# Optimization experiments

Hardware: AMD Instinct MI355X
Metric: run time of the kernel (lower is better)

Reference implementation:

```python
import jax, jax.numpy as jnp
import numpy as np

N = 50000      # nodes per graph batch (per side)
E = 600000     # edges per side
B = 4096       # number of graphs (drug pairs)
D = 128        # node_dim == hidden_dim
K = 128        # kge_dim
R = 86         # rel_total
L = 3          # n_iter
EPS = 1e-5


def setup_inputs() -> dict:
    key = jax.random.key(0)
    ks = jax.random.split(key, 16)
    inp = {}
    inp["x1"] = jax.random.normal(ks[0], (N, D), jnp.float32)
    inp["x2"] = jax.random.normal(ks[1], (N, D), jnp.float32)
    inp["edge_index1"] = jax.random.randint(ks[2], (2, E), 0, N)
    inp["edge_index2"] = jax.random.randint(ks[3], (2, E), 0, N)
    inp["batch1"] = jnp.sort(jax.random.randint(ks[4], (N,), 0, B))
    inp["batch2"] = jnp.sort(jax.random.randint(ks[5], (N,), 0, B))
    inp["rel"] = jax.random.randint(ks[6], (B,), 0, R)
    # SAGEConv params, stacked over L layers (all [D,D] since node_dim==hidden_dim)
    sc = 0.05
    inp["Wl"] = jax.random.normal(ks[7], (L, D, D), jnp.float32) * sc   # lin on aggregated neighbors (has bias)
    inp["bl"] = jnp.zeros((L, D), jnp.float32)
    inp["Wr"] = jax.random.normal(ks[8], (L, D, D), jnp.float32) * sc   # root (self) lin, no bias
    # BatchNorm (eval mode: running stats)
    inp["bn_gamma"] = jnp.ones((L, D), jnp.float32)
    inp["bn_beta"] = jnp.zeros((L, D), jnp.float32)
    inp["bn_mean"] = jnp.zeros((L, D), jnp.float32)
    inp["bn_var"] = jnp.ones((L, D), jnp.float32)
    # relation embedding + final MLP
    inp["kge"] = jax.random.normal(ks[9], (R, K), jnp.float32)
    inp["W1"] = jax.random.normal(ks[10], (2 * D + K, D), jnp.float32) * sc
    inp["b1"] = jnp.zeros((D,), jnp.float32)
    inp["W2"] = jax.random.normal(ks[11], (D, 1), jnp.float32) * sc
    inp["b2"] = jnp.zeros((1,), jnp.float32)
    return inp


def _gnn(x, edge_index, Wl, bl, Wr, g, b, m, v):
    src, dst = edge_index[0], edge_index[1]
    deg = jax.ops.segment_sum(jnp.ones((E,), x.dtype), dst, num_segments=N)
    deg = jnp.maximum(deg, 1.0)[:, None]
    for i in range(L):
        agg = jax.ops.segment_sum(x[src], dst, num_segments=N) / deg  # mean aggregation
        h = agg @ Wl[i] + bl[i] + x @ Wr[i]                           # SAGEConv
        h = (h - m[i]) * (g[i] / jnp.sqrt(v[i] + EPS)) + b[i]         # BN (eval)
        x = jax.nn.relu(h)                                            # dropout = identity (eval)
    return x


def reference(x1, edge_index1, batch1, x2, edge_index2, batch2, rel,
              Wl, bl, Wr, bn_gamma, bn_beta, bn_mean, bn_var,
              kge, W1, b1, W2, b2):
    h1 = _gnn(x1, edge_index1, Wl, bl, Wr, bn_gamma, bn_beta, bn_mean, bn_var)
    h2 = _gnn(x2, edge_index2, Wl, bl, Wr, bn_gamma, bn_beta, bn_mean, bn_var)
    p1 = jax.ops.segment_sum(h1, batch1, num_segments=B)  # global_add_pool
    p2 = jax.ops.segment_sum(h2, batch2, num_segments=B)
    r = kge[rel]                                          # [B, K]
    z = jnp.concatenate([p1, p2, r], axis=-1)             # [B, 2D+K]
    h = jax.nn.relu(z @ W1 + b1)
    out = h @ W2 + b2
    return out.reshape(-1)
```

## Files before the change

### kernel.cpp

```cpp
#include <hip/hip_runtime.h>

#define NN 50000
#define NE 600000
#define NB 4096
#define DD 128
#define EPSV 1e-5f
#define NBKT 196
#define NCHUNK 256
#define CHSZ ((NE + NCHUNK - 1) / NCHUNK)

typedef __bf16 bf16x8 __attribute__((ext_vector_type(8)));
typedef float f32x4 __attribute__((ext_vector_type(4)));
typedef float f32x2 __attribute__((ext_vector_type(2)));

__device__ inline unsigned short f2bf(float f) {
    unsigned u = __float_as_uint(f);
    u = (u + 0x7FFFu + ((u >> 16) & 1u)) >> 16;
    return (unsigned short)u;
}
__device__ inline float bf2f(unsigned short h) {
    return __uint_as_float(((unsigned)h) << 16);
}

__global__ void k_prep(const float* __restrict__ x1, const float* __restrict__ x2,
                       unsigned short* __restrict__ xh, unsigned short* __restrict__ xl,
                       const float* __restrict__ Wl, const float* __restrict__ Wr,
                       const float* __restrict__ W1,
                       unsigned short* __restrict__ wf, unsigned* __restrict__ w1p,
                       const int* __restrict__ d0, const int* __restrict__ d1,
                       int* __restrict__ bcnt) {
    __shared__ int h[NBKT];
    int b = blockIdx.x;
    int tid = threadIdx.x;
    if (b < 12500) {
        int i = b * 256 + tid;
        const float* x = (i < NN * 32) ? x1 : x2;
        int j = (i < NN * 32) ? i : i - NN * 32;
        float4 v = ((const float4*)x)[j];
        ushort4 hh, ll;
        hh.x = f2bf(v.x); ll.x = f2bf(v.x - bf2f(hh.x));
        hh.y = f2bf(v.y); ll.y = f2bf(v.y - bf2f(hh.y));
        hh.z = f2bf(v.z); ll.z = f2bf(v.z - bf2f(hh.z));
        hh.w = f2bf(v.w); ll.w = f2bf(v.w - bf2f(hh.w));
        ((ushort4*)xh)[i] = hh;
        ((ushort4*)xl)[i] = ll;
    } else if (b < 12500 + 576) {
        int t = (b - 12500) * 256 + tid;
        if (t < 3 * 128 * 256) {
            int k = t & 255;
            int n = (t >> 8) & 127;
            int l = t >> 15;
            float w = (k < 128) ? Wl[l * 16384 + k * 128 + n] : Wr[l * 16384 + (k - 128) * 128 + n];
            unsigned short hh = f2bf(w);
            unsigned short lo = f2bf(w - bf2f(hh));
            int ntile = n >> 4, fm = n & 15, kc = k >> 5, kq = (k & 31) >> 3, j = k & 7;
            size_t pos = (size_t)l * 65536 + (size_t)(ntile * 8 + kc) * 1024 +
                         (size_t)(kq * 16 + fm) * 8 + j;
            wf[pos] = hh;
            wf[pos + 512] = lo;
        } else if (t < 3 * 128 * 256 + 128 * 384) {
            int u = t - 3 * 128 * 256;
            int n = u / 384;
            int k = u - n * 384;
            float w = W1[k * 128 + n];
            unsigned short hh = f2bf(w);
            unsigned short ll = f2bf(w - bf2f(hh));
            w1p[u] = ((unsigned)hh << 16) | (unsigned)ll;
        }
    } else {
        int hb = b - 13076;
        int side = (hb >= NCHUNK) ? 1 : 0;
        int c = hb - side * NCHUNK;
        const int* dst = side ? d1 : d0;
        for (int i = tid; i < NBKT; i += 256) h[i] = 0;
        __syncthreads();
        int e0 = c * CHSZ, e1 = min(e0 + CHSZ, NE);
        for (int e = e0 + tid; e < e1; e += 256) atomicAdd(&h[dst[e] >> 8], 1);
        __syncthreads();
        int* bc = bcnt + ((size_t)side * NCHUNK + c) * NBKT;
        for (int i = tid; i < NBKT; i += 256) bc[i] = h[i];
    }
}

__global__ void k_s1(int* __restrict__ bcnt, int* __restrict__ btot) {
    int side = (blockIdx.x >= NBKT) ? 1 : 0;
    int b = blockIdx.x - side * NBKT;
    int tid = threadIdx.x;
    int idx = ((size_t)side * NCHUNK + tid) * NBKT + b;
    int v = bcnt[idx];
    int lane = tid & 63, wv = tid >> 6;
    int x = v;
#pragma unroll
    for (int off = 1; off < 64; off <<= 1) {
        int y = __shfl_up(x, off, 64);
        if (lane >= off) x += y;
    }
    __shared__ int ws4[4];
    if (lane == 63) ws4[wv] = x;
    __syncthreads();
    int add = 0;
#pragma unroll
    for (int w = 0; w < 4; w++)
        if (w < wv) add += ws4[w];
    int incl = x + add;
    bcnt[idx] = incl - v;
    if (tid == 255) btot[side * NBKT + b] = incl;
}

__global__ void k_s2(const int* __restrict__ btot, int* __restrict__ bbase,
                     int* __restrict__ ptrC) {
    int side = blockIdx.x;
    int tid = threadIdx.x;
    int v = (tid < NBKT) ? btot[side * NBKT + tid] : 0;
    int lane = tid & 63, wv = tid >> 6;
    int x = v;
#pragma unroll
    for (int off = 1; off < 64; off <<= 1) {
        int y = __shfl_up(x, off, 64);
        if (lane >= off) x += y;
    }
    __shared__ int ws4[4];
    if (lane == 63) ws4[wv] = x;
    __syncthreads();
    int add = 0;
#pragma unroll
    for (int w = 0; w < 4; w++)
        if (w < wv) add += ws4[w];
    int incl = x + add;
    if (tid < NBKT) bbase[side * NBKT + tid] = incl - v;
    if (tid == 0 && side == 1) ptrC[2 * NN] = 2 * NE;
}

__global__ void k_part(const int* __restrict__ s0, const int* __restrict__ d0,
                       const int* __restrict__ s1, const int* __restrict__ d1,
                       const int* __restrict__ bcnt, const int* __restrict__ bbase,
                       int* __restrict__ part) {
    int side = (blockIdx.x >= NCHUNK) ? 1 : 0;
    int c = blockIdx.x - side * NCHUNK;
    const int* src = side ? s1 : s0;
    const int* dst = side ? d1 : d0;
    int tid = threadIdx.x;
    __shared__ int off[NBKT];
    const int* bc = bcnt + ((size_t)side * NCHUNK + c) * NBKT;
    for (int i = tid; i < NBKT; i += 256) off[i] = bbase[side * NBKT + i] + bc[i];
    __syncthreads();
    int e0 = c * CHSZ, e1 = min(e0 + CHSZ, NE);
    int* P = part + (size_t)side * NE;
    int soff = side * NN;
    for (int e = e0 + tid; e < e1; e += 256) {
        int d = dst[e];
        int pos = atomicAdd(&off[d >> 8], 1);
        P[pos] = ((src[e] + soff) << 8) | (d & 255);
    }
}

__global__ void k_csr(const int* __restrict__ part, const int* __restrict__ bbase,
                      int* __restrict__ ptrC, float* __restrict__ invdC,
                      int* __restrict__ csrC) {
    int side = (blockIdx.x >= NBKT) ? 1 : 0;
    int b = blockIdx.x - side * NBKT;
    int tid = threadIdx.x;
    const int* P = part + (size_t)side * NE;
    int base = bbase[side * NBKT + b];
    int endp = (b == NBKT - 1) ? NE : bbase[side * NBKT + b + 1];
    __shared__ int cnt[256];
    cnt[tid] = 0;
    __syncthreads();
    for (int e = base + tid; e < endp; e += 256) atomicAdd(&cnt[P[e] & 255], 1);
    __syncthreads();
    int v = cnt[tid];
    int lane = tid & 63, wv = tid >> 6;
    int x = v;
#pragma unroll
    for (int off = 1; off < 64; off <<= 1) {
        int y = __shfl_up(x, off, 64);
        if (lane >= off) x += y;
    }
    __shared__ int ws4[4];
    if (lane == 63) ws4[wv] = x;
    __syncthreads();
    int add = 0;
#pragma unroll
    for (int w = 0; w < 4; w++)
        if (w < wv) add += ws4[w];
    int excl = x + add - v;
    int node = (b << 8) + tid;
    if (node < NN) {
        ptrC[side * NN + node] = side * NE + base + excl;
        invdC[side * NN + node] = 1.0f / (float)(v > 1 ? v : 1);
    }
    __syncthreads();
    cnt[tid] = excl;
    __syncthreads();
    for (int e = base + tid; e < endp; e += 256) {
        int p = P[e];
        int pos = atomicAdd(&cnt[p & 255], 1);
        csrC[(size_t)side * NE + base + pos] = p >> 8;
    }
}

__global__ void k_gather(const unsigned short* __restrict__ xh, const int* __restrict__ ptr,
                         const int* __restrict__ csr, const float* __restrict__ invd,
                         unsigned short* __restrict__ aggH) {
    int wid = threadIdx.x >> 6;
    int lane = threadIdx.x & 63;
    int q = lane >> 4;
    int c = lane & 15;
    int n = blockIdx.x * 4 + wid;
    if (n >= 2 * NN) return;
    int beg = ptr[n], end = ptr[n + 1];
    float id = invd[n];
    f32x2 a2[4];
#pragma unroll
    for (int k = 0; k < 4; k++) a2[k] = (f32x2){0.f, 0.f};

    for (int base = beg; base < end; base += 64) {
        int cnt = min(end - base, 64);
        int idxv = csr[base + min(lane, cnt - 1)];
        for (int e0 = 0; e0 < cnt; e0 += 16) {
            int eA = e0 + q, eB = e0 + 4 + q, eC = e0 + 8 + q, eD = e0 + 12 + q;
            int iA = __shfl(idxv, eA, 64);
            int iB = __shfl(idxv, eB, 64);
            int iC = __shfl(idxv, eC, 64);
            int iD = __shfl(idxv, eD, 64);
            f32x2 wA2 = (eA < cnt) ? (f32x2){1.f, 1.f} : (f32x2){0.f, 0.f};
            f32x2 wB2 = (eB < cnt) ? (f32x2){1.f, 1.f} : (f32x2){0.f, 0.f};
            f32x2 wC2 = (eC < cnt) ? (f32x2){1.f, 1.f} : (f32x2){0.f, 0.f};
            f32x2 wD2 = (eD < cnt) ? (f32x2){1.f, 1.f} : (f32x2){0.f, 0.f};
            uint4 vA = *(const uint4*)(xh + (((unsigned)iA << 7) + (c << 3)));
            uint4 vB = *(const uint4*)(xh + (((unsigned)iB << 7) + (c << 3)));
            uint4 vC = *(const uint4*)(xh + (((unsigned)iC << 7) + (c << 3)));
            uint4 vD = *(const uint4*)(xh + (((unsigned)iD << 7) + (c << 3)));
            a2[0] += wA2 * (f32x2){__uint_as_float(vA.x << 16), __uint_as_float(vA.x & 0xffff0000u)};
            a2[1] += wA2 * (f32x2){__uint_as_float(vA.y << 16), __uint_as_float(vA.y & 0xffff0000u)};
            a2[2] += wA2 * (f32x2){__uint_as_float(vA.z << 16), __uint_as_float(vA.z & 0xffff0000u)};
            a2[3] += wA2 * (f32x2){__uint_as_float(vA.w << 16), __uint_as_float(vA.w & 0xffff0000u)};
            a2[0] += wB2 * (f32x2){__uint_as_float(vB.x << 16), __uint_as_float(vB.x & 0xffff0000u)};
            a2[1] += wB2 * (f32x2){__uint_as_float(vB.y << 16), __uint_as_float(vB.y & 0xffff0000u)};
            a2[2] += wB2 * (f32x2){__uint_as_float(vB.z << 16), __uint_as_float(vB.z & 0xffff0000u)};
            a2[3] += wB2 * (f32x2){__uint_as_float(vB.w << 16), __uint_as_float(vB.w & 0xffff0000u)};
            a2[0] += wC2 * (f32x2){__uint_as_float(vC.x << 16), __uint_as_float(vC.x & 0xffff0000u)};
            a2[1] += wC2 * (f32x2){__uint_as_float(vC.y << 16), __uint_as_float(vC.y & 0xffff0000u)};
            a2[2] += wC2 * (f32x2){__uint_as_float(vC.z << 16), __uint_as_float(vC.z & 0xffff0000u)};
            a2[3] += wC2 * (f32x2){__uint_as_float(vC.w << 16), __uint_as_float(vC.w & 0xffff0000u)};
            a2[0] += wD2 * (f32x2){__uint_as_float(vD.x << 16), __uint_as_float(vD.x & 0xffff0000u)};
            a2[1] += wD2 * (f32x2){__uint_as_float(vD.y << 16), __uint_as_float(vD.y & 0xffff0000u)};
            a2[2] += wD2 * (f32x2){__uint_as_float(vD.z << 16), __uint_as_float(vD.z & 0xffff0000u)};
            a2[3] += wD2 * (f32x2){__uint_as_float(vD.w << 16), __uint_as_float(vD.w & 0xffff0000u)};
        }
    }
    float a[8];
    a[0] = a2[0][0]; a[1] = a2[0][1];
    a[2] = a2[1][0]; a[3] = a2[1][1];
    a[4] = a2[2][0]; a[5] = a2[2][1];
    a[6] = a2[3][0]; a[7] = a2[3][1];
#pragma unroll
    for (int k = 0; k < 8; k++) {
        a[k] += __shfl_xor(a[k], 16, 64);
        a[k] += __shfl_xor(a[k], 32, 64);
    }
    if (q == 0) {
        unsigned short h0 = f2bf(a[0] * id), h1 = f2bf(a[1] * id);
        unsigned short h2 = f2bf(a[2] * id), h3 = f2bf(a[3] * id);
        unsigned short h4 = f2bf(a[4] * id), h5 = f2bf(a[5] * id);
        unsigned short h6 = f2bf(a[6] * id), h7 = f2bf(a[7] * id);
        uint4 o;
        o.x = (unsigned)h0 | ((unsigned)h1 << 16);
        o.y = (unsigned)h2 | ((unsigned)h3 << 16);
        o.z = (unsigned)h4 | ((unsigned)h5 << 16);
        o.w = (unsigned)h6 | ((unsigned)h7 << 16);
        *(uint4*)(aggH + (size_t)n * DD + c * 8) = o;
    }
}

__launch_bounds__(256)
__global__ void k_gemmW(const unsigned short* __restrict__ AH,
                        const unsigned short* __restrict__ XH, const unsigned short* __restrict__ XL,
                        const unsigned short* __restrict__ wf,
                        const float* __restrict__ bl, const float* __restrict__ g,
                        const float* __restrict__ be, const float* __restrict__ mn,
                        const float* __restrict__ vr,
                        unsigned short* __restrict__ OH, unsigned short* __restrict__ OL,
                        float* __restrict__ Of, int f32out) {
    __shared__ __align__(16) unsigned short sBuf[8192];
    int tid = threadIdx.x;
    int lane = tid & 63, w = tid >> 6;
    int fm = lane & 15, kq = lane >> 4;
    int m0 = blockIdx.x * 64;
    int wr = (w & 1) * 32;
    int wn = (w >> 1) * 64;
    int ksw = kq ^ ((fm >> 1) & 3);

    int srow = tid >> 2, sseg = tid & 3;
    int ldsoff = srow * 32 + ((sseg ^ ((srow >> 1) & 3)) << 3);
    bool sok = (m0 + srow) < 2 * NN;
    size_t gbase = (size_t)(m0 + srow) * DD + sseg * 8;

    float scv[4], shv[4];
#pragma unroll
    for (int nt = 0; nt < 4; nt++) {
        int jj = wn + nt * 16 + fm;
        float s = g[jj] * rsqrtf(vr[jj] + EPSV);
        scv[nt] = s;
        shv[nt] = (bl[jj] - mn[jj]) * s + be[jj];
    }

    f32x4 acc[2][4];
#pragma unroll
    for (int i = 0; i < 2; i++)
#pragma unroll
        for (int j = 0; j < 4; j++) acc[i][j] = (f32x4){0.f, 0.f, 0.f, 0.f};

    const unsigned short* wfb = wf + (size_t)((w >> 1) * 4) * 8192 + lane * 8;

#pragma unroll
    for (int c = 0; c < 8; c++) {
        int isA = (c < 4);
        if (c > 0) __syncthreads();
        {
            uint4 av = make_uint4(0, 0, 0, 0), lv = make_uint4(0, 0, 0, 0);
            size_t gofs = gbase + (size_t)(c & 3) * 32;
            if (sok) {
                av = *(const uint4*)((isA ? AH : XH) + gofs);
                if (!isA) lv = *(const uint4*)(XL + gofs);
            }
            *(uint4*)&sBuf[ldsoff] = av;
            if (!isA) *(uint4*)&sBuf[2048 + ldsoff] = lv;
        }
        bf16x8 wh[4], wl[4];
#pragma unroll
        for (int nt = 0; nt < 4; nt++) {
            const unsigned short* p = wfb + (size_t)(nt * 8 + c) * 1024;
            wh[nt] = *(const bf16x8*)p;
            wl[nt] = *(const bf16x8*)(p + 512);
        }
        __syncthreads();

        bf16x8 ah[2], al[2];
#pragma unroll
        for (int mt = 0; mt < 2; mt++) {
            int r = wr + mt * 16 + fm;
            ah[mt] = *(const bf16x8*)&sBuf[r * 32 + ksw * 8];
            if (!isA) al[mt] = *(const bf16x8*)&sBuf[2048 + r * 32 + ksw * 8];
        }
#pragma unroll
        for (int nt = 0; nt < 4; nt++) {
#pragma unroll
            for (int mt = 0; mt < 2; mt++) {
                acc[mt][nt] = __builtin_amdgcn_mfma_f32_16x16x32_bf16(ah[mt], wh[nt], acc[mt][nt], 0, 0, 0);
                acc[mt][nt] = __builtin_amdgcn_mfma_f32_16x16x32_bf16(ah[mt], wl[nt], acc[mt][nt], 0, 0, 0);
                if (!isA)
                    acc[mt][nt] = __builtin_amdgcn_mfma_f32_16x16x32_bf16(al[mt], wh[nt], acc[mt][nt], 0, 0, 0);
            }
        }
    }

    unsigned* cb = (unsigned*)sBuf;
    int c8 = tid & 15;
    for (int h = 0; h < 2; h++) {
        __syncthreads();
        if ((w & 1) == h) {
#pragma unroll
            for (int mt = 0; mt < 2; mt++) {
#pragma unroll
                for (int r = 0; r < 4; r++) {
                    int rh = mt * 16 + kq * 4 + r;
#pragma unroll
                    for (int nt = 0; nt < 4; nt++) {
                        int col = wn + nt * 16 + fm;
                        float o = fmaxf(acc[mt][nt][r] * scv[nt] + shv[nt], 0.f);
                        unsigned pv;
                        if (f32out) {
                            pv = __float_as_uint(o);
                        } else {
                            unsigned short hi_ = f2bf(o);
                            pv = ((unsigned)hi_ << 16) | (unsigned)f2bf(o - bf2f(hi_));
                        }
                        cb[rh * 128 + col] = pv;
                    }
                }
            }
        }
        __syncthreads();
        if (f32out) {
#pragma unroll
            for (int j = 0; j < 4; j++) {
                int row = (tid >> 5) + j * 8;
                int grow = m0 + h * 32 + row;
                if (grow < 2 * NN)
                    *(uint4*)&Of[(size_t)grow * DD + (tid & 31) * 4] =
                        *(const uint4*)&cb[row * 128 + (tid & 31) * 4];
            }
        } else {
#pragma unroll
            for (int j = 0; j < 2; j++) {
                int row = (tid >> 4) + j * 16;
                int grow = m0 + h * 32 + row;
                if (grow < 2 * NN) {
                    const unsigned* u = &cb[row * 128 + c8 * 8];
                    uint4 hv, lv2;
                    hv.x = (u[0] >> 16) | (u[1] & 0xFFFF0000u);
                    hv.y = (u[2] >> 16) | (u[3] & 0xFFFF0000u);
                    hv.z = (u[4] >> 16) | (u[5] & 0xFFFF0000u);
                    hv.w = (u[6] >> 16) | (u[7] & 0xFFFF0000u);
                    lv2.x = (u[0] & 0xFFFFu) | (u[1] << 16);
                    lv2.y = (u[2] & 0xFFFFu) | (u[3] << 16);
                    lv2.z = (u[4] & 0xFFFFu) | (u[5] << 16);
                    lv2.w = (u[6] & 0xFFFFu) | (u[7] << 16);
                    *(uint4*)&OH[(size_t)grow * DD + c8 * 8] = hv;
                    *(uint4*)&OL[(size_t)grow * DD + c8 * 8] = lv2;
                }
            }
        }
    }
}

__launch_bounds__(128)
__global__ void k_pool2z(const float* __restrict__ cf, const int* __restrict__ bt1,
                         const int* __restrict__ bt2, const int* __restrict__ rel,
                         const float* __restrict__ kge,
                         unsigned short* __restrict__ zh, unsigned short* __restrict__ zl) {
    int side = (blockIdx.x >= NB) ? 1 : 0;
    int b = blockIdx.x - side * NB;
    const int* batch = side ? bt2 : bt1;
    const float* h = cf + (size_t)side * NN * DD;
    __shared__ int sr[2];
    if (threadIdx.x < 2) {
        int target = b + (int)threadIdx.x;
        int lo = 0, hi = NN;
        while (lo < hi) {
            int mid = (lo + hi) >> 1;
            if (batch[mid] < target) lo = mid + 1; else hi = mid;
        }
        sr[threadIdx.x] = lo;
    }
    __syncthreads();
    int beg = sr[0], end = sr[1];
    int t = threadIdx.x;
    float acc = 0.f;
    for (int r = beg; r < end; r++) acc += h[(size_t)r * DD + t];
    size_t zo = (size_t)b * 384 + side * 128 + t;
    unsigned short hh = f2bf(acc);
    zh[zo] = hh;
    zl[zo] = f2bf(acc - bf2f(hh));
    if (side == 0) {
        float kv = kge[(size_t)rel[b] * 128 + t];
        size_t zk = (size_t)b * 384 + 256 + t;
        unsigned short kh = f2bf(kv);
        zh[zk] = kh;
        zl[zk] = f2bf(kv - bf2f(kh));
    }
}

__launch_bounds__(256)
__global__ void k_mlp2(const unsigned short* __restrict__ zh, const unsigned short* __restrict__ zl,
                       const unsigned* __restrict__ w1p,
                       const float* __restrict__ b1, const float* __restrict__ W2,
                       const float* __restrict__ b2, float* __restrict__ out) {
    __shared__ __align__(16) unsigned short sZ[2][32 * 40];
    __shared__ __align__(16) unsigned short sW[2][128 * 40];
    __shared__ float hpart[32][4];
    int tid = threadIdx.x;
    int m0 = blockIdx.x * 32;
    int lane = tid & 63, w = tid >> 6;
    int fm = lane & 15, q = lane >> 4;
    int wn = w * 32;

    f32x4 acc[2][2];
#pragma unroll
    for (int i = 0; i < 2; i++)
#pragma unroll
        for (int j = 0; j < 2; j++) acc[i][j] = (f32x4){0.f, 0.f, 0.f, 0.f};

    for (int c = 0; c < 12; c++) {
        int k0 = c * 32;
        __syncthreads();
        {
            int row = tid >> 3, seg = tid & 7;
            size_t off = (size_t)(m0 + row) * 384 + k0 + seg * 4;
            *(ushort4*)&sZ[0][row * 40 + seg * 4] = *(const ushort4*)(zh + off);
            *(ushort4*)&sZ[1][row * 40 + seg * 4] = *(const ushort4*)(zl + off);
        }
#pragma unroll
        for (int i = 0; i < 4; i++) {
            int u = tid + 256 * i;
            int row = u >> 3, seg = u & 7;
            uint4 val = *(const uint4*)(w1p + (size_t)row * 384 + k0 + seg * 4);
            ushort4 hi, lo;
            hi.x = val.x >> 16; hi.y = val.y >> 16; hi.z = val.z >> 16; hi.w = val.w >> 16;
            lo.x = val.x & 0xFFFF; lo.y = val.y & 0xFFFF; lo.z = val.z & 0xFFFF; lo.w = val.w & 0xFFFF;
            *(ushort4*)&sW[0][row * 40 + seg * 4] = hi;
            *(ushort4*)&sW[1][row * 40 + seg * 4] = lo;
        }
        __syncthreads();
        bf16x8 zfh[2], zfl[2];
#pragma unroll
        for (int mt = 0; mt < 2; mt++) {
            int r = mt * 16 + fm;
            zfh[mt] = *(const bf16x8*)&sZ[0][r * 40 + q * 8];
            zfl[mt] = *(const bf16x8*)&sZ[1][r * 40 + q * 8];
        }
#pragma unroll
        for (int nt = 0; nt < 2; nt++) {
            int nr = wn + nt * 16 + fm;
            bf16x8 wh = *(const bf16x8*)&sW[0][nr * 40 + q * 8];
            bf16x8 wl = *(const bf16x8*)&sW[1][nr * 40 + q * 8];
#pragma unroll
            for (int mt = 0; mt < 2; mt++) {
                acc[mt][nt] = __builtin_amdgcn_mfma_f32_16x16x32_bf16(zfh[mt], wh, acc[mt][nt], 0, 0, 0);
                acc[mt][nt] = __builtin_amdgcn_mfma_f32_16x16x32_bf16(zfh[mt], wl, acc[mt][nt], 0, 0, 0);
                acc[mt][nt] = __builtin_amdgcn_mfma_f32_16x16x32_bf16(zfl[mt], wh, acc[mt][nt], 0, 0, 0);
            }
        }
    }

    float b1v[2], w2v[2];
#pragma unroll
    for (int nt = 0; nt < 2; nt++) {
        int col = wn + nt * 16 + fm;
        b1v[nt] = b1[col];
        w2v[nt] = W2[col];
    }
#pragma unroll
    for (int mt = 0; mt < 2; mt++) {
#pragma unroll
        for (int r = 0; r < 4; r++) {
            float val = 0.f;
#pragma unroll
            for (int nt = 0; nt < 2; nt++)
                val += fmaxf(acc[mt][nt][r] + b1v[nt], 0.f) * w2v[nt];
#pragma unroll
            for (int m = 1; m < 16; m <<= 1) val += __shfl_xor(val, m, 64);
            if (fm == 0) hpart[mt * 16 + q * 4 + r][w] = val;
        }
    }
    __syncthreads();
    if (tid < 32)
        out[m0 + tid] = hpart[tid][0] + hpart[tid][1] + hpart[tid][2] + hpart[tid][3] + b2[0];
}

extern "C" void kernel_launch(void* const* d_in, const int* in_sizes, int n_in,
                              void* d_out, int out_size, void* d_ws, size_t ws_size,
                              hipStream_t stream) {
    const float* x1  = (const float*)d_in[0];
    const float* x2  = (const float*)d_in[1];
    const int*   ei1 = (const int*)d_in[2];
    const int*   ei2 = (const int*)d_in[3];
    const int*   bt1 = (const int*)d_in[4];
    const int*   bt2 = (const int*)d_in[5];
    const int*   rel = (const int*)d_in[6];
    const float* Wl  = (const float*)d_in[7];
    const float* bl  = (const float*)d_in[8];
    const float* Wr  = (const float*)d_in[9];
    const float* g   = (const float*)d_in[10];
    const float* be  = (const float*)d_in[11];
    const float* mn  = (const float*)d_in[12];
    const float* vr  = (const float*)d_in[13];
    const float* kge = (const float*)d_in[14];
    const float* W1  = (const float*)d_in[15];
    const float* b1v = (const float*)d_in[16];
    const float* W2  = (const float*)d_in[17];
    const float* b2v = (const float*)d_in[18];

    char* ws = (char*)d_ws;
    size_t off = 0;
    auto alloc = [&](size_t bytes) {
        void* p = ws + off;
        off += (bytes + 255) & ~(size_t)255;
        return p;
    };
    const size_t PL = (size_t)2 * NN * DD;
    unsigned short* xbufH = (unsigned short*)alloc(PL * 2);
    unsigned short* xbufL = (unsigned short*)alloc(PL * 2);
    unsigned short* obufH = (unsigned short*)alloc(PL * 2);
    unsigned short* obufL = (unsigned short*)alloc(PL * 2);
    unsigned short* aggH  = (unsigned short*)alloc(PL * 2);
    unsigned short* wf    = (unsigned short*)alloc((size_t)3 * 65536 * 2);
    unsigned* w1p  = (unsigned*)alloc((size_t)128 * 384 * 4);
    unsigned short* zh = (unsigned short*)alloc((size_t)NB * 384 * 2);
    unsigned short* zl = (unsigned short*)alloc((size_t)NB * 384 * 2);
    int*   bcnt    = (int*)alloc((size_t)2 * NCHUNK * NBKT * 4);
    int*   btot    = (int*)alloc((size_t)2 * NBKT * 4);
    int*   bbase   = (int*)alloc((size_t)2 * NBKT * 4);
    int*   part    = (int*)alloc((size_t)2 * NE * 4);
    int*   ptrC    = (int*)alloc((size_t)(2 * NN + 1) * 4);
    float* invdC   = (float*)alloc((size_t)2 * NN * 4);
    int*   csrC    = (int*)alloc((size_t)2 * NE * 4);
    if (off > ws_size) return;

    float* cf = (float*)obufH;

    const int nbPrep  = 12500 + 576 + 512;
    const int nbNode4 = (2 * NN + 3) / 4;
    const int nbGemmW = (2 * NN + 63) / 64;

    k_prep<<<nbPrep, 256, 0, stream>>>(x1, x2, xbufH, xbufL, Wl, Wr, W1, wf, w1p,
                                       ei1 + NE, ei2 + NE, bcnt);

    k_s1<<<2 * NBKT, 256, 0, stream>>>(bcnt, btot);
    k_s2<<<2, 256, 0, stream>>>(btot, bbase, ptrC);
    k_part<<<2 * NCHUNK, 256, 0, stream>>>(ei1, ei1 + NE, ei2, ei2 + NE, bcnt, bbase, part);
    k_csr<<<2 * NBKT, 256, 0, stream>>>(part, bbase, ptrC, invdC, csrC);

    k_gather<<<nbNode4, 256, 0, stream>>>(xbufH, ptrC, csrC, invdC, aggH);
    k_gemmW<<<nbGemmW, 256, 0, stream>>>(aggH, xbufH, xbufL, wf, bl, g, be, mn, vr,
                                         obufH, obufL, (float*)nullptr, 0);
    k_gather<<<nbNode4, 256, 0, stream>>>(obufH, ptrC, csrC, invdC, aggH);
    k_gemmW<<<nbGemmW, 256, 0, stream>>>(aggH, obufH, obufL, wf + 65536, bl + 128, g + 128,
                                         be + 128, mn + 128, vr + 128,
                                         xbufH, xbufL, (float*)nullptr, 0);
    k_gather<<<nbNode4, 256, 0, stream>>>(xbufH, ptrC, csrC, invdC, aggH);
    k_gemmW<<<nbGemmW, 256, 0, stream>>>(aggH, xbufH, xbufL, wf + 131072, bl + 256, g + 256,
                                         be + 256, mn + 256, vr + 256,
                                         (unsigned short*)nullptr, (unsigned short*)nullptr, cf, 1);

    k_pool2z<<<2 * NB, 128, 0, stream>>>(cf, bt1, bt2, rel, kge, zh, zl);
    k_mlp2<<<NB / 32, 256, 0, stream>>>(zh, zl, w1p, b1v, W2, b2v, (float*)d_out);
}
```

Measured before the change: 420.3 us.

## Software-pipeline gather loads and widen GEMM LDS staging to 64-wide K chunks

The neighbor gather loop now prefetches the next group of four bf16 rows while it accumulates the current group, so global-load latency overlaps with the unpack-and-add work. The SAGE GEMM kernel stages 64 K-columns per LDS pass instead of 32, using a new 8-way XOR swizzle. This halves the number of barrier-separated stages from 8 to 4. The cost is more live registers in the gather kernel and double the LDS footprint per stage, which could lower occupancy.

```diff
diff --git a/kernel.cpp b/kernel.cpp
--- a/kernel.cpp
+++ b/kernel.cpp
@@ -199,6 +199,32 @@
     }
 }
 
+#define ONE2 ((f32x2){1.f, 1.f})
+#define ZERO2 ((f32x2){0.f, 0.f})
+#define UNP2H(u) __uint_as_float((u) << 16)
+#define UNP2L(u) __uint_as_float((u) & 0xffff0000u)
+#define LOADG(E0, VA, VB, VC, VD, WA, WB, WC, WD)                                  \
+    {                                                                              \
+        int eA_ = (E0) + q, eB_ = (E0) + 4 + q, eC_ = (E0) + 8 + q, eD_ = (E0) + 12 + q; \
+        int iA_ = __shfl(idxv, eA_, 64);                                           \
+        int iB_ = __shfl(idxv, eB_, 64);                                           \
+        int iC_ = __shfl(idxv, eC_, 64);                                           \
+        int iD_ = __shfl(idxv, eD_, 64);                                           \
+        WA = (eA_ < cnt) ? ONE2 : ZERO2;                                           \
+        WB = (eB_ < cnt) ? ONE2 : ZERO2;                                           \
+        WC = (eC_ < cnt) ? ONE2 : ZERO2;                                           \
+        WD = (eD_ < cnt) ? ONE2 : ZERO2;                                           \
+        VA = *(const uint4*)(xh + (((unsigned)iA_ << 7) + (c << 3)));              \
+        VB = *(const uint4*)(xh + (((unsigned)iB_ << 7) + (c << 3)));              \
+        VC = *(const uint4*)(xh + (((unsigned)iC_ << 7) + (c << 3)));              \
+        VD = *(const uint4*)(xh + (((unsigned)iD_ << 7) + (c << 3)));              \
+    }
+#define PROC1(V, W)                                                                \
+    a2[0] += W * (f32x2){UNP2H(V.x), UNP2L(V.x)};                                  \
+    a2[1] += W * (f32x2){UNP2H(V.y), UNP2L(V.y)};                                  \
+    a2[2] += W * (f32x2){UNP2H(V.z), UNP2L(V.z)};                                  \
+    a2[3] += W * (f32x2){UNP2H(V.w), UNP2L(V.w)};
+
 __global__ void k_gather(const unsigned short* __restrict__ xh, const int* __restrict__ ptr,
                          const int* __restrict__ csr, const float* __restrict__ invd,
                          unsigned short* __restrict__ aggH) {
@@ -212,41 +238,25 @@
     float id = invd[n];
     f32x2 a2[4];
 #pragma unroll
-    for (int k = 0; k < 4; k++) a2[k] = (f32x2){0.f, 0.f};
+    for (int k = 0; k < 4; k++) a2[k] = ZERO2;
 
     for (int base = beg; base < end; base += 64) {
         int cnt = min(end - base, 64);
         int idxv = csr[base + min(lane, cnt - 1)];
+        uint4 cA, cB, cC, cD, nA, nB, nC, nD;
+        f32x2 xA, xB, xC, xD, yA, yB, yC, yD;
+        LOADG(0, cA, cB, cC, cD, xA, xB, xC, xD);
         for (int e0 = 0; e0 < cnt; e0 += 16) {
-            int eA = e0 + q, eB = e0 + 4 + q, eC = e0 + 8 + q, eD = e0 + 12 + q;
-            int iA = __shfl(idxv, eA, 64);
-            int iB = __shfl(idxv, eB, 64);
-            int iC = __shfl(idxv, eC, 64);
-            int iD = __shfl(idxv, eD, 64);
-            f32x2 wA2 = (eA < cnt) ? (f32x2){1.f, 1.f} : (f32x2){0.f, 0.f};
-            f32x2 wB2 = (eB < cnt) ? (f32x2){1.f, 1.f} : (f32x2){0.f, 0.f};
-            f32x2 wC2 = (eC < cnt) ? (f32x2){1.f, 1.f} : (f32x2){0.f, 0.f};
-            f32x2 wD2 = (eD < cnt) ? (f32x2){1.f, 1.f} : (f32x2){0.f, 0.f};
-            uint4 vA = *(const uint4*)(xh + (((unsigned)iA << 7) + (c << 3)));
-            uint4 vB = *(const uint4*)(xh + (((unsigned)iB << 7) + (c << 3)));
-            uint4 vC = *(const uint4*)(xh + (((unsigned)iC << 7) + (c << 3)));
-            uint4 vD = *(const uint4*)(xh + (((unsigned)iD << 7) + (c << 3)));
-            a2[0] += wA2 * (f32x2){__uint_as_float(vA.x << 16), __uint_as_float(vA.x & 0xffff0000u)};
-            a2[1] += wA2 * (f32x2){__uint_as_float(vA.y << 16), __uint_as_float(vA.y & 0xffff0000u)};
-            a2[2] += wA2 * (f32x2){__uint_as_float(vA.z << 16), __uint_as_float(vA.z & 0xffff0000u)};
-            a2[3] += wA2 * (f32x2){__uint_as_float(vA.w << 16), __uint_as_float(vA.w & 0xffff0000u)};
-            a2[0] += wB2 * (f32x2){__uint_as_float(vB.x << 16), __uint_as_float(vB.x & 0xffff0000u)};
-            a2[1] += wB2 * (f32x2){__uint_as_float(vB.y << 16), __uint_as_float(vB.y & 0xffff0000u)};
-            a2[2] += wB2 * (f32x2){__uint_as_float(vB.z << 16), __uint_as_float(vB.z & 0xffff0000u)};
-            a2[3] += wB2 * (f32x2){__uint_as_float(vB.w << 16), __uint_as_float(vB.w & 0xffff0000u)};
-            a2[0] += wC2 * (f32x2){__uint_as_float(vC.x << 16), __uint_as_float(vC.x & 0xffff0000u)};
-            a2[1] += wC2 * (f32x2){__uint_as_float(vC.y << 16), __uint_as_float(vC.y & 0xffff0000u)};
-            a2[2] += wC2 * (f32x2){__uint_as_float(vC.z << 16), __uint_as_float(vC.z & 0xffff0000u)};
-            a2[3] += wC2 * (f32x2){__uint_as_float(vC.w << 16), __uint_as_float(vC.w & 0xffff0000u)};
-            a2[0] += wD2 * (f32x2){__uint_as_float(vD.x << 16), __uint_as_float(vD.x & 0xffff0000u)};
-            a2[1] += wD2 * (f32x2){__uint_as_float(vD.y << 16), __uint_as_float(vD.y & 0xffff0000u)};
-            a2[2] += wD2 * (f32x2){__uint_as_float(vD.z << 16), __uint_as_float(vD.z & 0xffff0000u)};
-            a2[3] += wD2 * (f32x2){__uint_as_float(vD.w << 16), __uint_as_float(vD.w & 0xffff0000u)};
+            bool more = (e0 + 16) < cnt;
+            if (more) LOADG(e0 + 16, nA, nB, nC, nD, yA, yB, yC, yD);
+            PROC1(cA, xA);
+            PROC1(cB, xB);
+            PROC1(cC, xC);
+            PROC1(cD, xD);
+            if (more) {
+                cA = nA; cB = nB; cC = nC; cD = nD;
+                xA = yA; xB = yB; xC = yC; xD = yD;
+            }
         }
     }
     float a[8];
@@ -289,12 +299,18 @@
     int m0 = blockIdx.x * 64;
     int wr = (w & 1) * 32;
     int wn = (w >> 1) * 64;
-    int ksw = kq ^ ((fm >> 1) & 3);
-
-    int srow = tid >> 2, sseg = tid & 3;
-    int ldsoff = srow * 32 + ((sseg ^ ((srow >> 1) & 3)) << 3);
-    bool sok = (m0 + srow) < 2 * NN;
-    size_t gbase = (size_t)(m0 + srow) * DD + sseg * 8;
+
+    int soff[2];
+    bool sok[2];
+    size_t gb[2];
+#pragma unroll
+    for (int i = 0; i < 2; i++) {
+        int s = tid + 256 * i;
+        int row = s >> 3, seg = s & 7;
+        soff[i] = row * 64 + ((seg ^ (row & 7)) << 3);
+        sok[i] = (m0 + row) < 2 * NN;
+        gb[i] = (size_t)(m0 + row) * DD + seg * 8;
+    }
 
     float scv[4], shv[4];
 #pragma unroll
@@ -312,45 +328,53 @@
         for (int j = 0; j < 4; j++) acc[i][j] = (f32x4){0.f, 0.f, 0.f, 0.f};
 
     const unsigned short* wfb = wf + (size_t)((w >> 1) * 4) * 8192 + lane * 8;
-
-#pragma unroll
-    for (int c = 0; c < 8; c++) {
-        int isA = (c < 4);
-        if (c > 0) __syncthreads();
-        {
+    int r0 = wr + fm, r1 = wr + 16 + fm;
+    int rx0 = (r0 & 7), rx1 = (r1 & 7);
+
+#pragma unroll
+    for (int p = 0; p < 4; p++) {
+        int isA = (p < 2);
+        if (p > 0) __syncthreads();
+#pragma unroll
+        for (int i = 0; i < 2; i++) {
             uint4 av = make_uint4(0, 0, 0, 0), lv = make_uint4(0, 0, 0, 0);
-            size_t gofs = gbase + (size_t)(c & 3) * 32;
-            if (sok) {
-                av = *(const uint4*)((isA ? AH : XH) + gofs);
-                if (!isA) lv = *(const uint4*)(XL + gofs);
-            }
-            *(uint4*)&sBuf[ldsoff] = av;
-            if (!isA) *(uint4*)&sBuf[2048 + ldsoff] = lv;
-        }
-        bf16x8 wh[4], wl[4];
-#pragma unroll
-        for (int nt = 0; nt < 4; nt++) {
-            const unsigned short* p = wfb + (size_t)(nt * 8 + c) * 1024;
-            wh[nt] = *(const bf16x8*)p;
-            wl[nt] = *(const bf16x8*)(p + 512);
+            size_t go = gb[i] + (size_t)(p & 1) * 64;
+            if (sok[i]) {
+                av = *(const uint4*)((isA ? AH : XH) + go);
+                if (!isA) lv = *(const uint4*)(XL + go);
+            }
+            *(uint4*)&sBuf[soff[i]] = av;
+            if (!isA) *(uint4*)&sBuf[4096 + soff[i]] = lv;
         }
         __syncthreads();
 
-        bf16x8 ah[2], al[2];
-#pragma unroll
-        for (int mt = 0; mt < 2; mt++) {
-            int r = wr + mt * 16 + fm;
-            ah[mt] = *(const bf16x8*)&sBuf[r * 32 + ksw * 8];
-            if (!isA) al[mt] = *(const bf16x8*)&sBuf[2048 + r * 32 + ksw * 8];
-        }
-#pragma unroll
-        for (int nt = 0; nt < 4; nt++) {
-#pragma unroll
-            for (int mt = 0; mt < 2; mt++) {
-                acc[mt][nt] = __builtin_amdgcn_mfma_f32_16x16x32_bf16(ah[mt], wh[nt], acc[mt][nt], 0, 0, 0);
-                acc[mt][nt] = __builtin_amdgcn_mfma_f32_16x16x32_bf16(ah[mt], wl[nt], acc[mt][nt], 0, 0, 0);
-                if (!isA)
-                    acc[mt][nt] = __builtin_amdgcn_mfma_f32_16x16x32_bf16(al[mt], wh[nt], acc[mt][nt], 0, 0, 0);
+#pragma unroll
+        for (int cc = 0; cc < 2; cc++) {
+            int ch = p * 2 + cc;
+            bf16x8 wh[4], wl[4];
+#pragma unroll
+            for (int nt = 0; nt < 4; nt++) {
+                const unsigned short* pw = wfb + (size_t)(nt * 8 + ch) * 1024;
+                wh[nt] = *(const bf16x8*)pw;
+                wl[nt] = *(const bf16x8*)(pw + 512);
+            }
+            int sl = cc * 4 + kq;
+            bf16x8 ah[2], al[2];
+            ah[0] = *(const bf16x8*)&sBuf[r0 * 64 + ((sl ^ rx0) << 3)];
+            ah[1] = *(const bf16x8*)&sBuf[r1 * 64 + ((sl ^ rx1) << 3)];
+            if (!isA) {
+                al[0] = *(const bf16x8*)&sBuf[4096 + r0 * 64 + ((sl ^ rx0) << 3)];
+                al[1] = *(const bf16x8*)&sBuf[4096 + r1 * 64 + ((sl ^ rx1) << 3)];
+            }
+#pragma unroll
+            for (int nt = 0; nt < 4; nt++) {
+#pragma unroll
+                for (int mt = 0; mt < 2; mt++) {
+                    acc[mt][nt] = __builtin_amdgcn_mfma_f32_16x16x32_bf16(ah[mt], wh[nt], acc[mt][nt], 0, 0, 0);
+                    acc[mt][nt] = __builtin_amdgcn_mfma_f32_16x16x32_bf16(ah[mt], wl[nt], acc[mt][nt], 0, 0, 0);
+                    if (!isA)
+                        acc[mt][nt] = __builtin_amdgcn_mfma_f32_16x16x32_bf16(al[mt], wh[nt], acc[mt][nt], 0, 0, 0);
+                }
             }
         }
     }
```

New measurement: 523.3 us. 1.24x slower.
